# Kernel optimization log

Hardware: AMD Instinct MI355X
Metric: run time of the kernel (lower is better)

## Reference

```python
import jax, jax.numpy as jnp
import numpy as np
from itertools import product

N_VOX = 100000
GRID = 128
KS = 3
K = KS ** 3
INC_MAX, OUTC_MAX = 64, 96
RUNTIME_INC, RUNTIME_OUTC = 48, 64


def _build_rulebook(rng):
    flat = rng.choice(GRID ** 3, size=N_VOX, replace=False).astype(np.int64)
    coords = np.stack(np.unravel_index(flat, (GRID, GRID, GRID)), axis=1)  # [N,3]
    # Dense lookup table: flat coord -> voxel index (or -1).
    table = np.full(GRID ** 3, -1, dtype=np.int32)
    table[flat] = np.arange(N_VOX, dtype=np.int32)
    offsets = np.array(list(product([-1, 0, 1], repeat=3)), dtype=np.int64)  # [27,3]
    idx = np.empty((K, N_VOX), dtype=np.int32)
    for k, off in enumerate(offsets):
        nb = coords + off  # stride=1, dilation=1
        valid = np.all((nb >= 0) & (nb < GRID), axis=1)
        nb_flat = (nb[:, 0] * GRID + nb[:, 1]) * GRID + nb[:, 2]
        nb_flat = np.where(valid, nb_flat, 0)
        idx[k] = np.where(valid, table[nb_flat], -1)
    return idx


def setup_inputs() -> dict:
    key = jax.random.key(0)
    kf, kw = jax.random.split(key)
    features = jax.random.normal(kf, (N_VOX, RUNTIME_INC), dtype=jnp.float32)
    # Full kernel param [K, inc_max, outc_max]; runtime-sliced inside reference.
    std = 1.0 / np.sqrt(INC_MAX * K)
    kernel = jax.random.uniform(kw, (K, INC_MAX, OUTC_MAX), dtype=jnp.float32,
                                minval=-std, maxval=std)
    idx = jnp.asarray(_build_rulebook(np.random.default_rng(0)))  # [K, N]
    return {"features": features, "kernel": kernel, "idx": idx,
            "runtime_inc": RUNTIME_INC, "runtime_outc": RUNTIME_OUTC}


def reference(features, kernel, idx, runtime_inc, runtime_outc):
    # Dynamic channel slicing (static Python ints -> jit friendly).
    w = kernel[:, :runtime_inc, :runtime_outc]          # [K, Ci, Co]
    mask = idx >= 0                                      # [K, N]
    safe = jnp.where(mask, idx, 0)
    # Gather -> per-offset GEMM -> accumulate (scatter is identity: out idx == n).
    gathered = features[safe] * mask[..., None].astype(features.dtype)  # [K, N, Ci]
    out = jnp.einsum('knc,kco->no', gathered, w)         # [N, Co]
    return out
```

## Files before the change

kernel.cpp:

```cpp
#include <hip/hip_runtime.h>
#include <hip/hip_bf16.h>


#define NVOX      100000
#define INC       48
#define INC_MAX   64
#define OUTC      64
#define OUTC_MAX  96
#define KOFF      27
#define BM        128
#define KPAD      64
#define LDSTR     88

typedef __attribute__((ext_vector_type(8))) short  short8;
typedef __attribute__((ext_vector_type(4))) float  floatx4;

__device__ __forceinline__ short f2bf(float f) {
    union { __hip_bfloat16 h; short s; } u;
    u.h = __float2bfloat16(f);
    return u.s;
}

__global__ void __launch_bounds__(256)
spconv_mfma(const float* __restrict__ feat,
            const float* __restrict__ wk,
            const int*   __restrict__ idx,
            float*       __restrict__ out)
{
    __shared__ short Asm[BM * LDSTR];
    __shared__ short Bsm[OUTC * LDSTR];

    const int tid  = threadIdx.x;
    const int m0   = blockIdx.x * BM;
    const int lane = tid & 63;
    const int wave = tid >> 6;
    const int quad = lane >> 4;
    const int l16  = lane & 15;

    for (int e = tid; e < BM * (KPAD - INC); e += 256) {
        int m = e >> 4, c = INC + (e & 15);
        Asm[m * LDSTR + c] = 0;
    }
    for (int e = tid; e < OUTC * (KPAD - INC); e += 256) {
        int o = e >> 4, c = INC + (e & 15);
        Bsm[o * LDSTR + c] = 0;
    }

    floatx4 acc[2][4];
    #pragma unroll
    for (int i = 0; i < 2; ++i)
        #pragma unroll
        for (int j = 0; j < 4; ++j)
            acc[i][j] = (floatx4){0.f, 0.f, 0.f, 0.f};

    const int a_m  = tid >> 1;
    const int a_c0 = (tid & 1) * 24;
    const int b_o  = tid & 63;
    const int b_cg = tid >> 6;

    for (int k = 0; k < KOFF; ++k) {
        __syncthreads();

        {
            int gm = m0 + a_m;
            int gi = (gm < NVOX) ? idx[k * NVOX + gm] : -1;
            short8 pack[3];
            if (gi >= 0) {
                const floatx4* src = (const floatx4*)(feat + gi * INC + a_c0);
                floatx4 f[6];
                #pragma unroll
                for (int t = 0; t < 6; ++t) f[t] = src[t];
                #pragma unroll
                for (int t = 0; t < 3; ++t)
                    #pragma unroll
                    for (int j = 0; j < 8; ++j)
                        pack[t][j] = f2bf(f[(t * 8 + j) >> 2][(t * 8 + j) & 3]);
            } else {
                #pragma unroll
                for (int t = 0; t < 3; ++t)
                    #pragma unroll
                    for (int j = 0; j < 8; ++j)
                        pack[t][j] = 0;
            }
            short8* dst = (short8*)&Asm[a_m * LDSTR + a_c0];
            dst[0] = pack[0]; dst[1] = pack[1]; dst[2] = pack[2];
        }

        if (b_cg < 3) {
            int c0 = b_cg * 16;
            const float* src = wk + k * (INC_MAX * OUTC_MAX) + c0 * OUTC_MAX + b_o;
            short8 pack[2];
            #pragma unroll
            for (int t = 0; t < 2; ++t)
                #pragma unroll
                for (int j = 0; j < 8; ++j)
                    pack[t][j] = f2bf(src[(t * 8 + j) * OUTC_MAX]);
            short8* dst = (short8*)&Bsm[b_o * LDSTR + c0];
            dst[0] = pack[0]; dst[1] = pack[1];
        }

        __syncthreads();

        const int rm = wave * 32;
        #pragma unroll
        for (int ks = 0; ks < 2; ++ks) {
            short8 a[2], b[4];
            #pragma unroll
            for (int mt = 0; mt < 2; ++mt)
                a[mt] = *(const short8*)&Asm[(rm + mt * 16 + l16) * LDSTR + ks * 32 + quad * 8];
            #pragma unroll
            for (int nt = 0; nt < 4; ++nt)
                b[nt] = *(const short8*)&Bsm[(nt * 16 + l16) * LDSTR + ks * 32 + quad * 8];
            #pragma unroll
            for (int mt = 0; mt < 2; ++mt)
                #pragma unroll
                for (int nt = 0; nt < 4; ++nt)
                    acc[mt][nt] = __builtin_amdgcn_mfma_f32_16x16x32_bf16(
                        a[mt], b[nt], acc[mt][nt], 0, 0, 0);
        }
    }

    const int rm = wave * 32;
    #pragma unroll
    for (int mt = 0; mt < 2; ++mt) {
        #pragma unroll
        for (int r = 0; r < 4; ++r) {
            int gm = m0 + rm + mt * 16 + quad * 4 + r;
            if (gm < NVOX) {
                #pragma unroll
                for (int nt = 0; nt < 4; ++nt)
                    out[gm * OUTC + nt * 16 + l16] = acc[mt][nt][r];
            }
        }
    }
}

extern "C" void kernel_launch(void* const* d_in, const int* in_sizes, int n_in,
                              void* d_out, int out_size, void* d_ws, size_t ws_size,
                              hipStream_t stream) {
    const float* feat = (const float*)d_in[0];
    const float* wk   = (const float*)d_in[1];
    const int*   idx  = (const int*)d_in[2];
    float* out = (float*)d_out;

    const int grid = (NVOX + BM - 1) / BM;
    spconv_mfma<<<grid, 256, 0, stream>>>(feat, wk, idx, out);
}
```

Before: 130.2 us.

## Pre-convert features/weights to bf16 and register-prefetch next offset gather

Adds a prep kernel that converts features and sliced, transposed weights to bf16 in the workspace, halving gather bytes and removing per-offset conversion in the main loop. The main kernel moves to 64-row tiles with 128 threads and prefetches the next offset's idx, features and weights into registers while the current offset's MFMAs run. It falls back to on-the-fly fp32 conversion when the workspace is too small. The cost is an extra launch plus a full pass over the features, more registers per thread, and smaller tiles that reload weights more often.

New measurement: 122.4 us. -6.0%, faster.

```diff
diff --git a/kernel.cpp b/kernel.cpp
--- a/kernel.cpp
+++ b/kernel.cpp
@@ -8,9 +8,12 @@
 #define OUTC      64
 #define OUTC_MAX  96
 #define KOFF      27
-#define BM        128
-#define KPAD      64
-#define LDSTR     88
+#define BM        64
+#define LDSTR     72
+#define W_ELEMS   (KOFF * OUTC * INC)
+#define FEAT_ELEMS (NVOX * INC)
+#define WS_NEED   ((size_t)(FEAT_ELEMS + W_ELEMS) * 2)
+#define FEAT_BLKS 2344
 
 typedef __attribute__((ext_vector_type(8))) short  short8;
 typedef __attribute__((ext_vector_type(4))) float  floatx4;
@@ -22,10 +25,34 @@
 }
 
 __global__ void __launch_bounds__(256)
-spconv_mfma(const float* __restrict__ feat,
-            const float* __restrict__ wk,
-            const int*   __restrict__ idx,
-            float*       __restrict__ out)
+prep_cvt(const float* __restrict__ feat, const float* __restrict__ wk,
+         short* __restrict__ featb, short* __restrict__ wtb)
+{
+    int b = blockIdx.x;
+    if (b < FEAT_BLKS) {
+        int t = b * 256 + threadIdx.x;
+        if (t < FEAT_ELEMS / 8) {
+            const floatx4* src = (const floatx4*)(feat + t * 8);
+            floatx4 f0 = src[0], f1 = src[1];
+            short8 p;
+            #pragma unroll
+            for (int j = 0; j < 4; ++j) { p[j] = f2bf(f0[j]); p[4 + j] = f2bf(f1[j]); }
+            *(short8*)(featb + t * 8) = p;
+        }
+    } else {
+        int t = (b - FEAT_BLKS) * 256 + threadIdx.x;
+        int c = t % INC;
+        int rest = t / INC;
+        int o = rest % OUTC;
+        int k = rest / OUTC;
+        wtb[t] = f2bf(wk[k * (INC_MAX * OUTC_MAX) + c * OUTC_MAX + o]);
+    }
+}
+
+template<bool PRE>
+__global__ void __launch_bounds__(128, 4)
+spconv_main(const void* __restrict__ featp, const void* __restrict__ wp,
+            const int* __restrict__ idx, float* __restrict__ out)
 {
     __shared__ short Asm[BM * LDSTR];
     __shared__ short Bsm[OUTC * LDSTR];
@@ -37,13 +64,11 @@
     const int quad = lane >> 4;
     const int l16  = lane & 15;
 
-    for (int e = tid; e < BM * (KPAD - INC); e += 256) {
-        int m = e >> 4, c = INC + (e & 15);
-        Asm[m * LDSTR + c] = 0;
-    }
-    for (int e = tid; e < OUTC * (KPAD - INC); e += 256) {
-        int o = e >> 4, c = INC + (e & 15);
-        Bsm[o * LDSTR + c] = 0;
+    {
+        short8 z = (short8){0, 0, 0, 0, 0, 0, 0, 0};
+        int r = tid >> 1, c0 = INC + (tid & 1) * 8;
+        *(short8*)&Asm[r * LDSTR + c0] = z;
+        *(short8*)&Bsm[r * LDSTR + c0] = z;
     }
 
     floatx4 acc[2][4];
@@ -53,50 +78,92 @@
         for (int j = 0; j < 4; ++j)
             acc[i][j] = (floatx4){0.f, 0.f, 0.f, 0.f};
 
-    const int a_m  = tid >> 1;
-    const int a_c0 = (tid & 1) * 24;
-    const int b_o  = tid & 63;
-    const int b_cg = tid >> 6;
+    const int row = tid >> 1;
+    const int c0  = (tid & 1) * 24;
+    const int gm  = m0 + row;
+    const bool mrow = (gm < NVOX);
+
+    int gi_cur = mrow ? idx[gm] : -1;
+    int gi_nxt = mrow ? idx[NVOX + gm] : -1;
+
+    short8  rA[3], rB[3];
+    floatx4 fA[6];
+    float   fB[24];
+
+    if (PRE) {
+        if (gi_cur >= 0) {
+            const short8* s = (const short8*)((const short*)featp + gi_cur * INC + c0);
+            rA[0] = s[0]; rA[1] = s[1]; rA[2] = s[2];
+        }
+        const short8* w = (const short8*)((const short*)wp + row * INC + c0);
+        rB[0] = w[0]; rB[1] = w[1]; rB[2] = w[2];
+    } else {
+        if (gi_cur >= 0) {
+            const floatx4* s = (const floatx4*)((const float*)featp + gi_cur * INC + c0);
+            #pragma unroll
+            for (int t = 0; t < 6; ++t) fA[t] = s[t];
+        }
+        const float* w = (const float*)wp;
+        #pragma unroll
+        for (int j = 0; j < 24; ++j) fB[j] = w[(c0 + j) * OUTC_MAX + row];
+    }
 
     for (int k = 0; k < KOFF; ++k) {
         __syncthreads();
 
-        {
-            int gm = m0 + a_m;
-            int gi = (gm < NVOX) ? idx[k * NVOX + gm] : -1;
-            short8 pack[3];
-            if (gi >= 0) {
-                const floatx4* src = (const floatx4*)(feat + gi * INC + a_c0);
-                floatx4 f[6];
-                #pragma unroll
-                for (int t = 0; t < 6; ++t) f[t] = src[t];
+        short8* dA = (short8*)&Asm[row * LDSTR + c0];
+        short8* dB = (short8*)&Bsm[row * LDSTR + c0];
+        if (PRE) {
+            if (gi_cur >= 0) { dA[0] = rA[0]; dA[1] = rA[1]; dA[2] = rA[2]; }
+            else {
+                short8 z = (short8){0, 0, 0, 0, 0, 0, 0, 0};
+                dA[0] = z; dA[1] = z; dA[2] = z;
+            }
+            dB[0] = rB[0]; dB[1] = rB[1]; dB[2] = rB[2];
+        } else {
+            short8 p[3];
+            if (gi_cur >= 0) {
                 #pragma unroll
                 for (int t = 0; t < 3; ++t)
                     #pragma unroll
                     for (int j = 0; j < 8; ++j)
-                        pack[t][j] = f2bf(f[(t * 8 + j) >> 2][(t * 8 + j) & 3]);
+                        p[t][j] = f2bf(fA[(t * 8 + j) >> 2][(t * 8 + j) & 3]);
             } else {
                 #pragma unroll
                 for (int t = 0; t < 3; ++t)
                     #pragma unroll
-                    for (int j = 0; j < 8; ++j)
-                        pack[t][j] = 0;
-            }
-            short8* dst = (short8*)&Asm[a_m * LDSTR + a_c0];
-            dst[0] = pack[0]; dst[1] = pack[1]; dst[2] = pack[2];
-        }
-
-        if (b_cg < 3) {
-            int c0 = b_cg * 16;
-            const float* src = wk + k * (INC_MAX * OUTC_MAX) + c0 * OUTC_MAX + b_o;
-            short8 pack[2];
-            #pragma unroll
-            for (int t = 0; t < 2; ++t)
-                #pragma unroll
-                for (int j = 0; j < 8; ++j)
-                    pack[t][j] = f2bf(src[(t * 8 + j) * OUTC_MAX]);
-            short8* dst = (short8*)&Bsm[b_o * LDSTR + c0];
-            dst[0] = pack[0]; dst[1] = pack[1];
+                    for (int j = 0; j < 8; ++j) p[t][j] = 0;
+            }
+            dA[0] = p[0]; dA[1] = p[1]; dA[2] = p[2];
+            short8 q[3];
+            #pragma unroll
+            for (int t = 0; t < 3; ++t)
+                #pragma unroll
+                for (int j = 0; j < 8; ++j) q[t][j] = f2bf(fB[t * 8 + j]);
+            dB[0] = q[0]; dB[1] = q[1]; dB[2] = q[2];
+        }
+
+        gi_cur = gi_nxt;
+        gi_nxt = (k + 2 < KOFF && mrow) ? idx[(k + 2) * NVOX + gm] : -1;
+        if (k + 1 < KOFF) {
+            if (PRE) {
+                if (gi_cur >= 0) {
+                    const short8* s = (const short8*)((const short*)featp + gi_cur * INC + c0);
+                    rA[0] = s[0]; rA[1] = s[1]; rA[2] = s[2];
+                }
+                const short8* w = (const short8*)((const short*)wp +
+                                  (k + 1) * (OUTC * INC) + row * INC + c0);
+                rB[0] = w[0]; rB[1] = w[1]; rB[2] = w[2];
+            } else {
+                if (gi_cur >= 0) {
+                    const floatx4* s = (const floatx4*)((const float*)featp + gi_cur * INC + c0);
+                    #pragma unroll
+                    for (int t = 0; t < 6; ++t) fA[t] = s[t];
+                }
+                const float* w = (const float*)wp + (k + 1) * (INC_MAX * OUTC_MAX);
+                #pragma unroll
+                for (int j = 0; j < 24; ++j) fB[j] = w[(c0 + j) * OUTC_MAX + row];
+            }
         }
 
         __syncthreads();
@@ -125,11 +192,11 @@
     for (int mt = 0; mt < 2; ++mt) {
         #pragma unroll
         for (int r = 0; r < 4; ++r) {
-            int gm = m0 + rm + mt * 16 + quad * 4 + r;
-            if (gm < NVOX) {
+            int g = m0 + rm + mt * 16 + quad * 4 + r;
+            if (g < NVOX) {
                 #pragma unroll
                 for (int nt = 0; nt < 4; ++nt)
-                    out[gm * OUTC + nt * 16 + l16] = acc[mt][nt][r];
+                    out[g * OUTC + nt * 16 + l16] = acc[mt][nt][r];
             }
         }
     }
@@ -144,5 +211,14 @@
     float* out = (float*)d_out;
 
     const int grid = (NVOX + BM - 1) / BM;
-    spconv_mfma<<<grid, 256, 0, stream>>>(feat, wk, idx, out);
-}
+
+    if (ws_size >= WS_NEED) {
+        short* featb = (short*)d_ws;
+        short* wtb   = featb + FEAT_ELEMS;
+        const int wblks = (W_ELEMS + 255) / 256;
+        prep_cvt<<<FEAT_BLKS + wblks, 256, 0, stream>>>(feat, wk, featb, wtb);
+        spconv_main<true><<<grid, 128, 0, stream>>>(featb, wtb, idx, out);
+    } else {
+        spconv_main<false><<<grid, 128, 0, stream>>>(feat, wk, idx, out);
+    }
+}
```

## Pre-convert features and weights to bf16, load MFMA operands directly without LDS

Applied to the files above, without the earlier changes.

Adds a prep kernel that converts the features and the weight slices to bf16 once, with the weights stored transposed and padded in a workspace. The main kernel drops shared memory and block barriers: each wave gathers its own rows straight into MFMA operand registers, with idx prefetched two offsets ahead and the A operands double-buffered. This removes per-block repeated fp32 conversion and LDS round-trips, at the cost of an extra kernel launch, workspace traffic and redundant weight loads from each wave. A fallback path does on-the-fly conversion when the workspace is too small.

Result: slower. 194.5 us (+49.4%).

```diff
diff --git a/kernel.cpp b/kernel.cpp
--- a/kernel.cpp
+++ b/kernel.cpp
@@ -2,15 +2,17 @@
 #include <hip/hip_bf16.h>
 
 
-#define NVOX      100000
-#define INC       48
-#define INC_MAX   64
-#define OUTC      64
-#define OUTC_MAX  96
-#define KOFF      27
-#define BM        128
-#define KPAD      64
-#define LDSTR     88
+#define NVOX       100000
+#define INC        48
+#define INC_MAX    64
+#define OUTC       64
+#define OUTC_MAX   96
+#define KOFF       27
+#define FEAT_ELEMS (NVOX * INC)
+#define WTB_ELEMS  (KOFF * OUTC * 64)
+#define FEAT_BLKS  2344
+#define WTB_BLKS   432
+#define WS_NEED    ((size_t)(FEAT_ELEMS + 64 + WTB_ELEMS) * 2)
 
 typedef __attribute__((ext_vector_type(8))) short  short8;
 typedef __attribute__((ext_vector_type(4))) float  floatx4;
@@ -22,29 +24,44 @@
 }
 
 __global__ void __launch_bounds__(256)
-spconv_mfma(const float* __restrict__ feat,
-            const float* __restrict__ wk,
-            const int*   __restrict__ idx,
-            float*       __restrict__ out)
+prep_cvt(const float* __restrict__ feat, const float* __restrict__ wk,
+         short* __restrict__ featb, short* __restrict__ wtb)
 {
-    __shared__ short Asm[BM * LDSTR];
-    __shared__ short Bsm[OUTC * LDSTR];
+    int b = blockIdx.x;
+    if (b < FEAT_BLKS) {
+        int t = b * 256 + threadIdx.x;
+        if (t < FEAT_ELEMS / 8) {
+            const floatx4* src = (const floatx4*)(feat + t * 8);
+            floatx4 f0 = src[0], f1 = src[1];
+            short8 p;
+            #pragma unroll
+            for (int j = 0; j < 4; ++j) { p[j] = f2bf(f0[j]); p[4 + j] = f2bf(f1[j]); }
+            *(short8*)(featb + t * 8) = p;
+        }
+    } else {
+        if (b == FEAT_BLKS && threadIdx.x < 64)
+            featb[FEAT_ELEMS + threadIdx.x] = 0;
+        int t = (b - FEAT_BLKS) * 256 + threadIdx.x;
+        int k = t >> 12, rem = t & 4095;
+        int o = rem >> 6, c = rem & 63;
+        wtb[t] = (c < INC) ? f2bf(wk[k * (INC_MAX * OUTC_MAX) + c * OUTC_MAX + o])
+                           : (short)0;
+    }
+}
 
-    const int tid  = threadIdx.x;
-    const int m0   = blockIdx.x * BM;
-    const int lane = tid & 63;
-    const int wave = tid >> 6;
+template<bool PRE>
+__global__ void __launch_bounds__(256, 4)
+spconv_direct(const void* __restrict__ featp, const void* __restrict__ wp,
+              const int* __restrict__ idx, float* __restrict__ out)
+{
+    const int lane = threadIdx.x & 63;
+    const int wave = threadIdx.x >> 6;
     const int quad = lane >> 4;
     const int l16  = lane & 15;
-
-    for (int e = tid; e < BM * (KPAD - INC); e += 256) {
-        int m = e >> 4, c = INC + (e & 15);
-        Asm[m * LDSTR + c] = 0;
-    }
-    for (int e = tid; e < OUTC * (KPAD - INC); e += 256) {
-        int o = e >> 4, c = INC + (e & 15);
-        Bsm[o * LDSTR + c] = 0;
-    }
+    const int m0   = (blockIdx.x * 4 + wave) * 32;
+    const int r0   = m0 + l16;
+    const int r1   = m0 + 16 + l16;
+    const bool v0  = r0 < NVOX, v1 = r1 < NVOX;
 
     floatx4 acc[2][4];
     #pragma unroll
@@ -53,83 +70,99 @@
         for (int j = 0; j < 4; ++j)
             acc[i][j] = (floatx4){0.f, 0.f, 0.f, 0.f};
 
-    const int a_m  = tid >> 1;
-    const int a_c0 = (tid & 1) * 24;
-    const int b_o  = tid & 63;
-    const int b_cg = tid >> 6;
+    short8 a[2][2][2];
+    const short8 z8 = (short8){0, 0, 0, 0, 0, 0, 0, 0};
 
+    auto aload = [&](short8 (*dst)[2], int g0, int g1) {
+        if (PRE) {
+            const short* fb = (const short*)featp;
+            const short8* p0 = (const short8*)(fb + (g0 < 0 ? 0 : g0) * INC + quad * 8);
+            const short8* p1 = (const short8*)(fb + (g1 < 0 ? 0 : g1) * INC + quad * 8);
+            short8 t00 = p0[0], t01 = p0[4];
+            short8 t10 = p1[0], t11 = p1[4];
+            dst[0][0] = (g0 < 0) ? z8 : t00;  dst[0][1] = (g0 < 0) ? z8 : t01;
+            dst[1][0] = (g1 < 0) ? z8 : t10;  dst[1][1] = (g1 < 0) ? z8 : t11;
+        } else {
+            const float* ff = (const float*)featp;
+            #pragma unroll
+            for (int mt = 0; mt < 2; ++mt) {
+                int g = mt ? g1 : g0;
+                const float* row = ff + (g < 0 ? 0 : g) * INC + quad * 8;
+                short8 s0, s1;
+                #pragma unroll
+                for (int j = 0; j < 8; ++j) s0[j] = f2bf(row[j]);
+                if (quad < 2) {
+                    #pragma unroll
+                    for (int j = 0; j < 8; ++j) s1[j] = f2bf(row[32 + j]);
+                } else s1 = z8;
+                dst[mt][0] = (g < 0) ? z8 : s0;
+                dst[mt][1] = (g < 0) ? z8 : s1;
+            }
+        }
+    };
+
+    int g0c = v0 ? idx[r0] : -1;
+    int g1c = v1 ? idx[r1] : -1;
+    int g0n = v0 ? idx[NVOX + r0] : -1;
+    int g1n = v1 ? idx[NVOX + r1] : -1;
+    aload(a[0], g0c, g1c);
+
+    #pragma unroll
     for (int k = 0; k < KOFF; ++k) {
-        __syncthreads();
+        int g0f = -1, g1f = -1;
+        if (k + 2 < KOFF) {
+            g0f = v0 ? idx[(k + 2) * NVOX + r0] : -1;
+            g1f = v1 ? idx[(k + 2) * NVOX + r1] : -1;
+        }
+        if (k + 1 < KOFF) aload(a[(k + 1) & 1], g0n, g1n);
 
-        {
-            int gm = m0 + a_m;
-            int gi = (gm < NVOX) ? idx[k * NVOX + gm] : -1;
-            short8 pack[3];
-            if (gi >= 0) {
-                const floatx4* src = (const floatx4*)(feat + gi * INC + a_c0);
-                floatx4 f[6];
+        short8 b[2][4];
+        if (PRE) {
+            const short8* wb = (const short8*)((const short*)wp +
+                               k * (OUTC * 64) + l16 * 64 + quad * 8);
+            #pragma unroll
+            for (int ks = 0; ks < 2; ++ks)
                 #pragma unroll
-                for (int t = 0; t < 6; ++t) f[t] = src[t];
+                for (int nt = 0; nt < 4; ++nt)
+                    b[ks][nt] = wb[nt * 128 + ks * 4];
+        } else {
+            const float* w = (const float*)wp + k * (INC_MAX * OUTC_MAX);
+            #pragma unroll
+            for (int ks = 0; ks < 2; ++ks)
                 #pragma unroll
-                for (int t = 0; t < 3; ++t)
+                for (int nt = 0; nt < 4; ++nt) {
+                    short8 f;
                     #pragma unroll
-                    for (int j = 0; j < 8; ++j)
-                        pack[t][j] = f2bf(f[(t * 8 + j) >> 2][(t * 8 + j) & 3]);
-            } else {
-                #pragma unroll
-                for (int t = 0; t < 3; ++t)
-                    #pragma unroll
-                    for (int j = 0; j < 8; ++j)
-                        pack[t][j] = 0;
-            }
-            short8* dst = (short8*)&Asm[a_m * LDSTR + a_c0];
-            dst[0] = pack[0]; dst[1] = pack[1]; dst[2] = pack[2];
+                    for (int j = 0; j < 8; ++j) {
+                        int c = ks * 32 + quad * 8 + j;
+                        f[j] = (c < INC) ? f2bf(w[c * OUTC_MAX + nt * 16 + l16])
+                                         : (short)0;
+                    }
+                    b[ks][nt] = f;
+                }
         }
 
-        if (b_cg < 3) {
-            int c0 = b_cg * 16;
-            const float* src = wk + k * (INC_MAX * OUTC_MAX) + c0 * OUTC_MAX + b_o;
-            short8 pack[2];
-            #pragma unroll
-            for (int t = 0; t < 2; ++t)
-                #pragma unroll
-                for (int j = 0; j < 8; ++j)
-                    pack[t][j] = f2bf(src[(t * 8 + j) * OUTC_MAX]);
-            short8* dst = (short8*)&Bsm[b_o * LDSTR + c0];
-            dst[0] = pack[0]; dst[1] = pack[1];
-        }
-
-        __syncthreads();
-
-        const int rm = wave * 32;
         #pragma unroll
-        for (int ks = 0; ks < 2; ++ks) {
-            short8 a[2], b[4];
-            #pragma unroll
-            for (int mt = 0; mt < 2; ++mt)
-                a[mt] = *(const short8*)&Asm[(rm + mt * 16 + l16) * LDSTR + ks * 32 + quad * 8];
-            #pragma unroll
-            for (int nt = 0; nt < 4; ++nt)
-                b[nt] = *(const short8*)&Bsm[(nt * 16 + l16) * LDSTR + ks * 32 + quad * 8];
+        for (int ks = 0; ks < 2; ++ks)
             #pragma unroll
             for (int mt = 0; mt < 2; ++mt)
                 #pragma unroll
                 for (int nt = 0; nt < 4; ++nt)
                     acc[mt][nt] = __builtin_amdgcn_mfma_f32_16x16x32_bf16(
-                        a[mt], b[nt], acc[mt][nt], 0, 0, 0);
-        }
+                        a[k & 1][mt][ks], b[ks][nt], acc[mt][nt], 0, 0, 0);
+
+        g0n = g0f; g1n = g1f;
     }
 
-    const int rm = wave * 32;
     #pragma unroll
     for (int mt = 0; mt < 2; ++mt) {
+        int gbase = m0 + mt * 16 + quad * 4;
         #pragma unroll
         for (int r = 0; r < 4; ++r) {
-            int gm = m0 + rm + mt * 16 + quad * 4 + r;
-            if (gm < NVOX) {
+            if (gbase + r < NVOX) {
                 #pragma unroll
                 for (int nt = 0; nt < 4; ++nt)
-                    out[gm * OUTC + nt * 16 + l16] = acc[mt][nt][r];
+                    out[(gbase + r) * OUTC + nt * 16 + l16] = acc[mt][nt][r];
             }
         }
     }
@@ -143,6 +176,15 @@
     const int*   idx  = (const int*)d_in[2];
     float* out = (float*)d_out;
 
-    const int grid = (NVOX + BM - 1) / BM;
-    spconv_mfma<<<grid, 256, 0, stream>>>(feat, wk, idx, out);
+    const int nwaves = NVOX / 32;
+    const int grid   = (nwaves + 3) / 4;
+
+    if (ws_size >= WS_NEED) {
+        short* featb = (short*)d_ws;
+        short* wtb   = featb + FEAT_ELEMS + 64;
+        prep_cvt<<<FEAT_BLKS + WTB_BLKS, 256, 0, stream>>>(feat, wk, featb, wtb);
+        spconv_direct<true><<<grid, 256, 0, stream>>>(featb, wtb, idx, out);
+    } else {
+        spconv_direct<false><<<grid, 256, 0, stream>>>(feat, wk, idx, out);
+    }
 }
```
